# Performance work log

Hardware: AMD Instinct MI355X
Metric: run time of the kernel (lower is better)

The kernel has to match this reference:

```python
import jax, jax.numpy as jnp
import numpy as np
import math

NUM_HEADS = 8
LN_EPS = 1e-5


def layer_norm(x, g, b):
    mu = x.mean(-1, keepdims=True)
    var = ((x - mu) ** 2).mean(-1, keepdims=True)
    return (x - mu) * jax.lax.rsqrt(var + LN_EPS) * g + b


def typed_linear(x, W, types):
    # x: [E, in], W: [R, in, out], types: [E] int -> [E, out]
    out = jnp.zeros((x.shape[0], W.shape[-1]), x.dtype)
    for r in range(W.shape[0]):  # small fixed relation count
        out = out + jnp.where((types == r)[:, None], x @ W[r], 0.0)
    return out


def setup_inputs() -> dict:
    key = jax.random.key(0)
    ks = jax.random.split(key, 20)
    N, M, E = 50000, 10000, 100000
    in_dim, e_dim, out_dim, td = 128, 32, 128, 32
    R, T = 8, 4
    inp = {
        'src_h': jax.random.normal(ks[0], (N, in_dim), jnp.float32),
        'src_tw': jax.random.normal(ks[1], (N, td), jnp.float32),
        'src_tb': jax.random.normal(ks[2], (N, td), jnp.float32),
        'edge_h': jax.random.normal(ks[3], (E, e_dim), jnp.float32),
        'date': jax.random.uniform(ks[4], (E,), jnp.float32),
        'src_idx': jax.random.randint(ks[5], (E,), 0, N, jnp.int32),
        'dst_idx': jax.random.randint(ks[6], (E,), 0, M, jnp.int32),
        'etype': jax.random.randint(ks[7], (E,), 0, R, jnp.int32),
        'ntype': jax.random.randint(ks[8], (M,), 0, T, jnp.int32),
    }
    def w(k, shape):
        return jax.random.normal(k, shape, jnp.float32) / math.sqrt(shape[-2])
    inp['Wq'] = w(ks[9], (R, in_dim, out_dim))
    inp['Wk'] = w(ks[10], (R, in_dim + e_dim, out_dim))
    inp['Wv'] = w(ks[11], (R, in_dim + e_dim, out_dim))
    inp['Wa'] = w(ks[12], (T, out_dim, out_dim))
    inp['h_bias'] = jnp.zeros((T, out_dim), jnp.float32)
    inp['skip'] = jnp.ones((T,), jnp.float32)
    inp['src_ln_g'] = jnp.ones((in_dim + e_dim,), jnp.float32)
    inp['src_ln_b'] = jnp.zeros((in_dim + e_dim,), jnp.float32)
    inp['dst_ln_g'] = jnp.ones((in_dim,), jnp.float32)
    inp['dst_ln_b'] = jnp.zeros((in_dim,), jnp.float32)
    return inp


def reference(src_h, src_tw, src_tb, edge_h, date, src_idx, dst_idx, etype, ntype,
              Wq, Wk, Wv, Wa, h_bias, skip, src_ln_g, src_ln_b, dst_ln_g, dst_ln_b):
    M = ntype.shape[0]
    out_dim = Wq.shape[-1]
    H = NUM_HEADS
    hs = out_dim // H
    td = src_tw.shape[-1]
    t = date[:, None]  # [E,1]

    # gather src / dst node data per edge (dst nodes are first M src rows)
    h_s, tw_s, tb_s = src_h[src_idx], src_tw[src_idx], src_tb[src_idx]
    h_d, tw_d, tb_d = src_h[dst_idx], src_tw[dst_idx], src_tb[dst_idx]

    # time2vec modulation of the first td channels
    dia_s = jnp.concatenate([jnp.sin(tw_s * t + tb_s) * h_s[:, :td], h_s[:, td:]], -1)
    dia_d = jnp.concatenate([jnp.sin(tw_d * t + tb_d) * h_d[:, :td], h_d[:, td:]], -1)
    dia_s = jnp.concatenate([dia_s, edge_h], -1)  # [E, in_dim+e_dim]

    # pre_norm
    dia_s = layer_norm(dia_s, src_ln_g, src_ln_b)
    dia_d = layer_norm(dia_d, dst_ln_g, dst_ln_b)

    q = typed_linear(dia_d, Wq, etype).reshape(-1, H, hs)
    k = typed_linear(dia_s, Wk, etype).reshape(-1, H, hs)
    v = typed_linear(dia_s, Wv, etype).reshape(-1, H, hs)

    a = (q * k).sum(-1) / math.sqrt(out_dim)  # [E, H]

    # edge_softmax: segment softmax over destination nodes
    amax = jax.lax.stop_gradient(jax.ops.segment_max(a, dst_idx, num_segments=M))
    ex = jnp.exp(a - amax[dst_idx])
    denom = jax.ops.segment_sum(ex, dst_idx, num_segments=M)
    alpha = ex / denom[dst_idx]  # [E, H]

    # weighted scatter-sum aggregation
    m = (v * alpha[..., None]).reshape(-1, out_dim)  # [E, out_dim]
    h = jax.ops.segment_sum(m, dst_idx, num_segments=M)  # [M, out_dim]

    h = h + h_bias[ntype]
    gate = jax.nn.sigmoid(skip[ntype])[:, None]
    h = typed_linear(h, Wa, ntype)  # dropout is identity at eval
    dst_h = src_h[:M]
    return h * gate + dst_h * (1.0 - gate)
```

## Files before the change

### kernel.cpp

```cpp
#include <hip/hip_runtime.h>


typedef __attribute__((ext_vector_type(8))) short short8;
typedef __attribute__((ext_vector_type(4))) float f32x4;

__device__ __forceinline__ unsigned short f2bf(float f){
  union { float f; unsigned u; } x; x.f = f;
  unsigned r = x.u + 0x7FFFu + ((x.u >> 16) & 1u);
  return (unsigned short)(r >> 16);
}
__device__ __forceinline__ float bf2f(unsigned short b){
  union { unsigned u; float f; } x; x.u = ((unsigned)b) << 16;
  return x.f;
}


__global__ void k_zero(int* __restrict__ p, int n){
  int i = blockIdx.x*256 + threadIdx.x;
  if(i < n) p[i] = 0;
}

__global__ __launch_bounds__(256) void k_hist(
    const int* __restrict__ etype, const int* __restrict__ dst_idx,
    const int* __restrict__ ntype,
    int* cnt_e, int* cnt_d, int* cnt_n, int E, int M){
  __shared__ int le[8], ln[4];
  int tid = threadIdx.x;
  if(tid < 8) le[tid] = 0;
  if(tid < 4) ln[tid] = 0;
  __syncthreads();
  int g = blockIdx.x*256 + tid;
  if(g < E){ atomicAdd(&le[etype[g]], 1); atomicAdd(&cnt_d[dst_idx[g]], 1); }
  if(g < M){ atomicAdd(&ln[ntype[g]], 1); }
  __syncthreads();
  if(tid < 8 && le[tid]) atomicAdd(&cnt_e[tid], le[tid]);
  if(tid < 4 && ln[tid]) atomicAdd(&cnt_n[tid], ln[tid]);
}

__global__ __launch_bounds__(1024) void k_scan(const int* __restrict__ cnt_e, int* off_e,
                                               const int* __restrict__ cnt_n, int* off_n,
                                               const int* __restrict__ cnt_d, int* off_d, int M){
  __shared__ int part[1024];
  int tid = threadIdx.x;
  if(tid == 0){
    int s = 0;
    for(int i=0;i<8;i++){ off_e[i]=s; s+=cnt_e[i]; } off_e[8]=s;
    s = 0;
    for(int i=0;i<4;i++){ off_n[i]=s; s+=cnt_n[i]; } off_n[4]=s;
  }
  int per = (M + 1023) >> 10;
  int s = 0;
  for(int j=0;j<per;j++){ int idx = tid*per + j; if(idx < M) s += cnt_d[idx]; }
  part[tid] = s; __syncthreads();
  for(int o=1;o<1024;o<<=1){
    int v = (tid >= o) ? part[tid-o] : 0;
    __syncthreads();
    part[tid] += v;
    __syncthreads();
  }
  int run = (tid == 0) ? 0 : part[tid-1];
  for(int j=0;j<per;j++){
    int idx = tid*per + j;
    if(idx < M){ off_d[idx] = run; run += cnt_d[idx]; }
  }
  if(tid == 1023) off_d[M] = run;
}

__global__ __launch_bounds__(256) void k_scatter(
    const int* __restrict__ etype, const int* __restrict__ dst_idx,
    const int* __restrict__ ntype,
    const int* __restrict__ off_e, int* cur_e,
    const int* __restrict__ off_d, int* cur_d,
    const int* __restrict__ off_n, int* cur_n,
    int* eperm, int* dstlist, int* nperm, int* npos, int E, int M){
  __shared__ int lcnt[8], lbase[8], lnc[4], lnb[4];
  int tid = threadIdx.x;
  if(tid < 8) lcnt[tid] = 0;
  if(tid < 4) lnc[tid] = 0;
  __syncthreads();
  int g = blockIdx.x*256 + tid;
  int r = 0, lrank = 0, t = 0, nrank = 0;
  bool inE = (g < E), inM = (g < M);
  if(inE){ r = etype[g]; lrank = atomicAdd(&lcnt[r], 1); }
  if(inM){ t = ntype[g]; nrank = atomicAdd(&lnc[t], 1); }
  __syncthreads();
  if(tid < 8 && lcnt[tid]) lbase[tid] = atomicAdd(&cur_e[tid], lcnt[tid]);
  if(tid < 4 && lnc[tid])  lnb[tid]   = atomicAdd(&cur_n[tid], lnc[tid]);
  __syncthreads();
  if(inE){
    int p = off_e[r] + lbase[r] + lrank;
    eperm[p] = g;
    int d = dst_idx[g];
    int q = off_d[d] + atomicAdd(&cur_d[d], 1);
    dstlist[q] = p;
  }
  if(inM){
    int np = off_n[t] + lnb[t] + nrank;
    npos[g] = np;
    nperm[np] = g;
  }
}

__global__ void k_convw(const float* __restrict__ Wq, const float* __restrict__ Wk,
                        const float* __restrict__ Wv, const float* __restrict__ Wa,
                        unsigned short* Wq_t, unsigned short* Wk_t,
                        unsigned short* Wv_t, unsigned short* Wa_t){
  int tid = blockIdx.x*256 + threadIdx.x;
  if(tid < 131072){
    int r = tid >> 14, rem = tid & 16383, k = rem >> 7, n = rem & 127;
    int nb=n>>4, m=n&15, c=k>>5, quad=(k>>3)&3, j=k&7;
    Wq_t[r*16384 + ((nb*4 + c)*4 + quad)*128 + m*8 + j] = f2bf(Wq[tid]);
  } else if(tid < 294912){
    int u = tid - 131072;
    int r = u / 20480, rem = u - r*20480, k = rem >> 7, n = rem & 127;
    int nb=n>>4, m=n&15, c=k>>5, quad=(k>>3)&3, j=k&7;
    Wk_t[r*20480 + ((nb*5 + c)*4 + quad)*128 + m*8 + j] = f2bf(Wk[u]);
  } else if(tid < 458752){
    int u = tid - 294912;
    int r = u / 20480, rem = u - r*20480, k = rem >> 7, n = rem & 127;
    int nb=n>>4, m=n&15, c=k>>5, quad=(k>>3)&3, j=k&7;
    Wv_t[r*20480 + ((nb*5 + c)*4 + quad)*128 + m*8 + j] = f2bf(Wv[u]);
  } else if(tid < 524288){
    int u = tid - 458752;
    int r = u >> 14, rem = u & 16383, k = rem >> 7, n = rem & 127;
    int nb=n>>4, m=n&15, c=k>>5, quad=(k>>3)&3, j=k&7;
    Wa_t[r*16384 + ((nb*4 + c)*4 + quad)*128 + m*8 + j] = f2bf(Wa[u]);
  }
}

__global__ __launch_bounds__(256) void k_prep(
  const float* __restrict__ src_h, const float* __restrict__ src_tw, const float* __restrict__ src_tb,
  const float* __restrict__ edge_h, const float* __restrict__ date,
  const int* __restrict__ src_idx, const int* __restrict__ dst_idx, const int* __restrict__ eperm,
  const float* __restrict__ g_s, const float* __restrict__ b_s,
  const float* __restrict__ g_d, const float* __restrict__ b_d,
  unsigned short* __restrict__ dia_s, unsigned short* __restrict__ dia_d, int E)
{
  int p = blockIdx.x*8 + (threadIdx.x >> 5);
  if(p >= E) return;
  int l = threadIdx.x & 31;
  int e = eperm[p];
  float t = date[e];
  int s = src_idx[e], d = dst_idx[e];
  float4 hs = *(const float4*)(src_h + (size_t)s*128 + 4*l);
  float4 hd = *(const float4*)(src_h + (size_t)d*128 + 4*l);
  float xe = edge_h[(size_t)e*32 + l];
  float4 sx = hs, dx = hd;
  if(l < 8){
    float4 w4, c4;
    w4 = *(const float4*)(src_tw + (size_t)s*32 + 4*l);
    c4 = *(const float4*)(src_tb + (size_t)s*32 + 4*l);
    sx.x = __sinf(w4.x*t + c4.x) * hs.x;
    sx.y = __sinf(w4.y*t + c4.y) * hs.y;
    sx.z = __sinf(w4.z*t + c4.z) * hs.z;
    sx.w = __sinf(w4.w*t + c4.w) * hs.w;
    w4 = *(const float4*)(src_tw + (size_t)d*32 + 4*l);
    c4 = *(const float4*)(src_tb + (size_t)d*32 + 4*l);
    dx.x = __sinf(w4.x*t + c4.x) * hd.x;
    dx.y = __sinf(w4.y*t + c4.y) * hd.y;
    dx.z = __sinf(w4.z*t + c4.z) * hd.z;
    dx.w = __sinf(w4.w*t + c4.w) * hd.w;
  }
  float s1 = sx.x + sx.y + sx.z + sx.w + xe;
  float s2 = sx.x*sx.x + sx.y*sx.y + sx.z*sx.z + sx.w*sx.w + xe*xe;
  float t1 = dx.x + dx.y + dx.z + dx.w;
  float t2 = dx.x*dx.x + dx.y*dx.y + dx.z*dx.z + dx.w*dx.w;
  #pragma unroll
  for(int i=1;i<32;i<<=1){
    s1 += __shfl_xor(s1,i); s2 += __shfl_xor(s2,i);
    t1 += __shfl_xor(t1,i); t2 += __shfl_xor(t2,i);
  }
  float smu = s1*(1.f/160.f);
  float ssc = rsqrtf(s2*(1.f/160.f) - smu*smu + 1e-5f);
  float dmu = t1*(1.f/128.f);
  float dsc = rsqrtf(t2*(1.f/128.f) - dmu*dmu + 1e-5f);
  float4 gs = *(const float4*)(g_s + 4*l), bs = *(const float4*)(b_s + 4*l);
  float4 gd = *(const float4*)(g_d + 4*l), bd = *(const float4*)(b_d + 4*l);
  unsigned r0 = (unsigned)f2bf((sx.x-smu)*ssc*gs.x + bs.x)
              | ((unsigned)f2bf((sx.y-smu)*ssc*gs.y + bs.y) << 16);
  unsigned r1 = (unsigned)f2bf((sx.z-smu)*ssc*gs.z + bs.z)
              | ((unsigned)f2bf((sx.w-smu)*ssc*gs.w + bs.w) << 16);
  uint2 rs; rs.x = r0; rs.y = r1;
  *(uint2*)(dia_s + (size_t)p*160 + 4*l) = rs;
  dia_s[(size_t)p*160 + 128 + l] = f2bf((xe-smu)*ssc*g_s[128+l] + b_s[128+l]);
  unsigned d0 = (unsigned)f2bf((dx.x-dmu)*dsc*gd.x + bd.x)
              | ((unsigned)f2bf((dx.y-dmu)*dsc*gd.y + bd.y) << 16);
  unsigned d1 = (unsigned)f2bf((dx.z-dmu)*dsc*gd.z + bd.z)
              | ((unsigned)f2bf((dx.w-dmu)*dsc*gd.w + bd.w) << 16);
  uint2 rd; rd.x = d0; rd.y = d1;
  *(uint2*)(dia_d + (size_t)p*128 + 4*l) = rd;
}

template<int NC>
__device__ __forceinline__ void gemm64r(
  const unsigned short* __restrict__ A, int lda,
  const unsigned short* __restrict__ Wf,
  f32x4* acc, int tid)
{
  int lane = tid & 63, w = tid >> 6, m = lane & 15, quad = lane >> 4;
  const unsigned short* p0 = Wf + (size_t)(2*w)*NC*512 + lane*8;
  short8 b0[NC], b1[NC];
  #pragma unroll
  for(int c=0;c<NC;c++){
    b0[c] = *(const short8*)(p0 + c*512);
    b1[c] = *(const short8*)(p0 + NC*512 + c*512);
  }
  #pragma unroll
  for(int i=0;i<8;i++) acc[i] = (f32x4){0.f,0.f,0.f,0.f};
  #pragma unroll
  for(int c=0;c<NC;c++){
    #pragma unroll
    for(int rt=0; rt<4; rt++){
      short8 af = *(const short8*)(A + (rt*16 + m)*lda + c*32 + quad*8);
      acc[rt*2+0] = __builtin_amdgcn_mfma_f32_16x16x32_bf16(af, b0[c], acc[rt*2+0], 0,0,0);
      acc[rt*2+1] = __builtin_amdgcn_mfma_f32_16x16x32_bf16(af, b1[c], acc[rt*2+1], 0,0,0);
    }
  }
}

__global__ __launch_bounds__(256) void k_qkv(
  const unsigned short* __restrict__ dia_d, const unsigned short* __restrict__ dia_s,
  const unsigned short* __restrict__ Wq_t, const unsigned short* __restrict__ Wk_t,
  const unsigned short* __restrict__ Wv_t,
  const int* __restrict__ cnt_e, const int* __restrict__ off_e,
  float* __restrict__ abuf, unsigned short* __restrict__ vbuf)
{
  __shared__ unsigned short Ad[64*136];
  __shared__ unsigned short As[64*168];
  int bid = blockIdx.x;
  int r = -1, tl0 = 0, accT = 0;
  #pragma unroll
  for(int i=0;i<8;i++){
    int n = cnt_e[i], tt = (n + 63) >> 6;
    if(r < 0 && bid < accT + tt){ r = i; tl0 = bid - accT; }
    accT += tt;
  }
  if(r < 0) return;
  int row0 = off_e[r] + tl0*64;
  int nv = min(64, cnt_e[r] - tl0*64);
  int tid = threadIdx.x;
  {
    int4 z = make_int4(0,0,0,0);
    #pragma unroll
    for(int it=0; it<4; it++){
      int idx = it*256 + tid, row = idx >> 4, c = idx & 15;
      int4 v = z;
      if(row < nv) v = *(const int4*)(dia_d + (size_t)(row0+row)*128 + c*8);
      *(int4*)(Ad + row*136 + c*8) = v;
    }
    #pragma unroll
    for(int it=0; it<5; it++){
      int idx = it*256 + tid, row = idx/20, c = idx%20;
      int4 v = z;
      if(row < nv) v = *(const int4*)(dia_s + (size_t)(row0+row)*160 + c*8);
      *(int4*)(As + row*168 + c*8) = v;
    }
  }
  __syncthreads();
  int lane = tid & 63, w = tid >> 6, m = lane & 15, quad = lane >> 4;
  f32x4 q[8], kk[8], vv[8];
  gemm64r<4>(Ad, 136, Wq_t + r*16384, q,  tid);
  gemm64r<5>(As, 168, Wk_t + r*20480, kk, tid);
  const float inv = 0.08838834764831845f;
  #pragma unroll
  for(int rt=0; rt<4; rt++)
  #pragma unroll
  for(int ct=0; ct<2; ct++){
    #pragma unroll
    for(int reg=0; reg<4; reg++){
      float s = q[rt*2+ct][reg] * kk[rt*2+ct][reg];
      s += __shfl_xor(s,1); s += __shfl_xor(s,2); s += __shfl_xor(s,4); s += __shfl_xor(s,8);
      int row = rt*16 + quad*4 + reg;
      if(m == 0 && row < nv) abuf[(size_t)(row0+row)*8 + w*2 + ct] = s * inv;
    }
  }
  gemm64r<5>(As, 168, Wv_t + r*20480, vv, tid);
  #pragma unroll
  for(int rt=0; rt<4; rt++)
  #pragma unroll
  for(int ct=0; ct<2; ct++)
  #pragma unroll
  for(int reg=0; reg<4; reg++){
    int row = rt*16 + quad*4 + reg;
    if(row < nv)
      vbuf[(size_t)(row0+row)*128 + w*32 + ct*16 + m] = f2bf(vv[rt*2+ct][reg]);
  }
}

__global__ __launch_bounds__(128) void k_aggr(
  const float* __restrict__ abuf, const unsigned short* __restrict__ vbuf,
  const int* __restrict__ dstlist, const int* __restrict__ off_d,
  const int* __restrict__ npos, const int* __restrict__ ntype,
  const float* __restrict__ h_bias, unsigned short* __restrict__ hpre)
{
  int d = blockIdx.x, tid = threadIdx.x;
  int o0 = off_d[d], cnt = off_d[d+1] - o0;
  __shared__ float den[8];
  if(tid < 8) den[tid] = 0.f;
  __syncthreads();
  for(int idx = tid; idx < cnt*8; idx += 128){
    int i = idx >> 3, h = idx & 7;
    float ex = __expf(abuf[(size_t)dstlist[o0+i]*8 + h]);
    atomicAdd(&den[h], ex);
  }
  __syncthreads();
  int h = tid >> 4;
  float dh = den[h];
  float rd = (dh > 0.f) ? (1.f/dh) : 0.f;
  float acc = 0.f;
  for(int i=0; i<cnt; i++){
    int p = dstlist[o0+i];
    float al = __expf(abuf[(size_t)p*8 + h]) * rd;
    acc += al * bf2f(vbuf[(size_t)p*128 + tid]);
  }
  int t = ntype[d];
  acc += h_bias[t*128 + tid];
  hpre[(size_t)npos[d]*128 + tid] = f2bf(acc);
}

__global__ __launch_bounds__(256) void k_final(
  const unsigned short* __restrict__ hpre, const unsigned short* __restrict__ Wa_t,
  const int* __restrict__ cnt_n, const int* __restrict__ off_n, const int* __restrict__ nperm,
  const float* __restrict__ skip, const float* __restrict__ src_h, float* __restrict__ out)
{
  __shared__ unsigned short Ah[64*136];
  int bid = blockIdx.x;
  int r = -1, tl0 = 0, accT = 0;
  #pragma unroll
  for(int i=0;i<4;i++){
    int n = cnt_n[i], tt = (n + 63) >> 6;
    if(r < 0 && bid < accT + tt){ r = i; tl0 = bid - accT; }
    accT += tt;
  }
  if(r < 0) return;
  int row0 = off_n[r] + tl0*64;
  int nv = min(64, cnt_n[r] - tl0*64);
  float gate = 1.f / (1.f + __expf(-skip[r]));
  int tid = threadIdx.x;
  int4 z = make_int4(0,0,0,0);
  #pragma unroll
  for(int it=0; it<4; it++){
    int idx = it*256 + tid, row = idx >> 4, c = idx & 15;
    int4 v = z;
    if(row < nv) v = *(const int4*)(hpre + (size_t)(row0+row)*128 + c*8);
    *(int4*)(Ah + row*136 + c*8) = v;
  }
  __syncthreads();
  f32x4 acc[8];
  gemm64r<4>(Ah, 136, Wa_t + r*16384, acc, tid);
  int lane = tid & 63, w = tid >> 6, m = lane & 15, quad = lane >> 4;
  #pragma unroll
  for(int rt=0; rt<4; rt++)
  #pragma unroll
  for(int ct=0; ct<2; ct++)
  #pragma unroll
  for(int reg=0; reg<4; reg++){
    int row = rt*16 + quad*4 + reg;
    if(row < nv){
      int dd = nperm[row0+row];
      int col = w*32 + ct*16 + m;
      out[(size_t)dd*128 + col] = acc[rt*2+ct][reg]*gate + src_h[(size_t)dd*128 + col]*(1.f - gate);
    }
  }
}

extern "C" void kernel_launch(void* const* d_in, const int* in_sizes, int n_in,
                              void* d_out, int out_size, void* d_ws, size_t ws_size,
                              hipStream_t stream)
{
  const float* src_h  = (const float*)d_in[0];
  const float* src_tw = (const float*)d_in[1];
  const float* src_tb = (const float*)d_in[2];
  const float* edge_h = (const float*)d_in[3];
  const float* date   = (const float*)d_in[4];
  const int*   src_idx= (const int*)d_in[5];
  const int*   dst_idx= (const int*)d_in[6];
  const int*   etype  = (const int*)d_in[7];
  const int*   ntype  = (const int*)d_in[8];
  const float* Wq     = (const float*)d_in[9];
  const float* Wk     = (const float*)d_in[10];
  const float* Wv     = (const float*)d_in[11];
  const float* Wa     = (const float*)d_in[12];
  const float* h_bias = (const float*)d_in[13];
  const float* skip   = (const float*)d_in[14];
  const float* g_s    = (const float*)d_in[15];
  const float* b_s    = (const float*)d_in[16];
  const float* g_d    = (const float*)d_in[17];
  const float* b_d    = (const float*)d_in[18];
  float* out = (float*)d_out;

  const int E = in_sizes[4];
  const int M = in_sizes[8];

  char* base = (char*)d_ws;
  size_t off = 0;
  auto alloc = [&](size_t bytes)->char*{
    off = (off + 255) & ~(size_t)255;
    char* p = base + off; off += bytes; return p;
  };
  int* cnt_e = (int*)alloc((size_t)(24 + 2*M)*4);
  int* cur_e = cnt_e + 8;
  int* cnt_n = cur_e + 8;
  int* cur_n = cnt_n + 4;
  int* cnt_d = cur_n + 4;
  int* cur_d = cnt_d + M;
  const int nzero = 24 + 2*M;
  int* off_e = (int*)alloc(9*4);
  int* off_n = (int*)alloc(5*4);
  int* off_d = (int*)alloc((size_t)(M+1)*4);
  int* eperm   = (int*)alloc((size_t)E*4);
  int* dstlist = (int*)alloc((size_t)E*4);
  int* nperm   = (int*)alloc((size_t)M*4);
  int* npos    = (int*)alloc((size_t)M*4);
  unsigned short* Wq_t = (unsigned short*)alloc((size_t)8*128*128*2);
  unsigned short* Wk_t = (unsigned short*)alloc((size_t)8*160*128*2);
  unsigned short* Wv_t = (unsigned short*)alloc((size_t)8*160*128*2);
  unsigned short* Wa_t = (unsigned short*)alloc((size_t)4*128*128*2);
  unsigned short* dia_d = (unsigned short*)alloc((size_t)E*128*2);
  unsigned short* dia_s = (unsigned short*)alloc((size_t)E*160*2);
  unsigned short* vbuf  = (unsigned short*)alloc((size_t)E*128*2);
  unsigned short* hpre  = (unsigned short*)alloc((size_t)M*128*2);
  float* abuf = (float*)alloc((size_t)E*8*4);

  k_zero<<<dim3((nzero+255)/256), dim3(256), 0, stream>>>(cnt_e, nzero);
  k_hist<<<dim3((E+255)/256), dim3(256), 0, stream>>>(etype, dst_idx, ntype, cnt_e, cnt_d, cnt_n, E, M);
  k_scan<<<dim3(1), dim3(1024), 0, stream>>>(cnt_e, off_e, cnt_n, off_n, cnt_d, off_d, M);
  k_scatter<<<dim3((E+255)/256), dim3(256), 0, stream>>>(etype, dst_idx, ntype,
      off_e, cur_e, off_d, cur_d, off_n, cur_n, eperm, dstlist, nperm, npos, E, M);
  k_convw<<<dim3(2048), dim3(256), 0, stream>>>(Wq, Wk, Wv, Wa, Wq_t, Wk_t, Wv_t, Wa_t);
  k_prep<<<dim3((E+7)/8), dim3(256), 0, stream>>>(src_h, src_tw, src_tb, edge_h, date,
      src_idx, dst_idx, eperm, g_s, b_s, g_d, b_d, dia_s, dia_d, E);
  k_qkv<<<dim3(E/64 + 9), dim3(256), 0, stream>>>(dia_d, dia_s, Wq_t, Wk_t, Wv_t,
      cnt_e, off_e, abuf, vbuf);
  k_aggr<<<dim3(M), dim3(128), 0, stream>>>(abuf, vbuf, dstlist, off_d, npos, ntype, h_bias, hpre);
  k_final<<<dim3(M/64 + 5), dim3(256), 0, stream>>>(hpre, Wa_t, cnt_n, off_n, nperm, skip, src_h, out);
}
```

Before: 269.0 us.

## Split typed GEMMs across eight waves, one 16-column head per wave

The q/k/v and final typed-linear kernels move from 256 threads per 64-row tile to 512. Each of the eight waves now computes one 16-column slice (one attention head) instead of two. This halves the accumulator and weight registers per wave and doubles the waves available to hide MFMA and LDS latency. The cost is that the A-tile fragments in shared memory are read by twice as many waves, with less reuse of each A load per MFMA. The head score now goes straight to abuf at index w, since the wave index equals the head.

Measured after the change: 264.6 us. About the same (-1.7%).

```diff
diff --git a/kernel.cpp b/kernel.cpp
--- a/kernel.cpp
+++ b/kernel.cpp
@@ -192,33 +192,29 @@
 }
 
 template<int NC>
-__device__ __forceinline__ void gemm64r(
+__device__ __forceinline__ void gemm64r8(
   const unsigned short* __restrict__ A, int lda,
   const unsigned short* __restrict__ Wf,
   f32x4* acc, int tid)
 {
   int lane = tid & 63, w = tid >> 6, m = lane & 15, quad = lane >> 4;
-  const unsigned short* p0 = Wf + (size_t)(2*w)*NC*512 + lane*8;
-  short8 b0[NC], b1[NC];
-  #pragma unroll
-  for(int c=0;c<NC;c++){
-    b0[c] = *(const short8*)(p0 + c*512);
-    b1[c] = *(const short8*)(p0 + NC*512 + c*512);
-  }
-  #pragma unroll
-  for(int i=0;i<8;i++) acc[i] = (f32x4){0.f,0.f,0.f,0.f};
+  const unsigned short* p0 = Wf + (size_t)w*NC*512 + lane*8;
+  short8 b0[NC];
+  #pragma unroll
+  for(int c=0;c<NC;c++) b0[c] = *(const short8*)(p0 + c*512);
+  #pragma unroll
+  for(int i=0;i<4;i++) acc[i] = (f32x4){0.f,0.f,0.f,0.f};
   #pragma unroll
   for(int c=0;c<NC;c++){
     #pragma unroll
     for(int rt=0; rt<4; rt++){
       short8 af = *(const short8*)(A + (rt*16 + m)*lda + c*32 + quad*8);
-      acc[rt*2+0] = __builtin_amdgcn_mfma_f32_16x16x32_bf16(af, b0[c], acc[rt*2+0], 0,0,0);
-      acc[rt*2+1] = __builtin_amdgcn_mfma_f32_16x16x32_bf16(af, b1[c], acc[rt*2+1], 0,0,0);
+      acc[rt] = __builtin_amdgcn_mfma_f32_16x16x32_bf16(af, b0[c], acc[rt], 0,0,0);
     }
   }
 }
 
-__global__ __launch_bounds__(256) void k_qkv(
+__global__ __launch_bounds__(512) void k_qkv(
   const unsigned short* __restrict__ dia_d, const unsigned short* __restrict__ dia_s,
   const unsigned short* __restrict__ Wq_t, const unsigned short* __restrict__ Wk_t,
   const unsigned short* __restrict__ Wv_t,
@@ -242,48 +238,47 @@
   {
     int4 z = make_int4(0,0,0,0);
     #pragma unroll
-    for(int it=0; it<4; it++){
-      int idx = it*256 + tid, row = idx >> 4, c = idx & 15;
+    for(int it=0; it<2; it++){
+      int idx = it*512 + tid, row = idx >> 4, c = idx & 15;
       int4 v = z;
       if(row < nv) v = *(const int4*)(dia_d + (size_t)(row0+row)*128 + c*8);
       *(int4*)(Ad + row*136 + c*8) = v;
     }
     #pragma unroll
-    for(int it=0; it<5; it++){
-      int idx = it*256 + tid, row = idx/20, c = idx%20;
-      int4 v = z;
-      if(row < nv) v = *(const int4*)(dia_s + (size_t)(row0+row)*160 + c*8);
-      *(int4*)(As + row*168 + c*8) = v;
+    for(int it=0; it<3; it++){
+      int idx = it*512 + tid;
+      if(idx < 1280){
+        int row = idx/20, c = idx%20;
+        int4 v = z;
+        if(row < nv) v = *(const int4*)(dia_s + (size_t)(row0+row)*160 + c*8);
+        *(int4*)(As + row*168 + c*8) = v;
+      }
     }
   }
   __syncthreads();
   int lane = tid & 63, w = tid >> 6, m = lane & 15, quad = lane >> 4;
-  f32x4 q[8], kk[8], vv[8];
-  gemm64r<4>(Ad, 136, Wq_t + r*16384, q,  tid);
-  gemm64r<5>(As, 168, Wk_t + r*20480, kk, tid);
+  f32x4 q[4], kk[4], vv[4];
+  gemm64r8<4>(Ad, 136, Wq_t + r*16384, q,  tid);
+  gemm64r8<5>(As, 168, Wk_t + r*20480, kk, tid);
   const float inv = 0.08838834764831845f;
   #pragma unroll
-  for(int rt=0; rt<4; rt++)
-  #pragma unroll
-  for(int ct=0; ct<2; ct++){
+  for(int rt=0; rt<4; rt++){
     #pragma unroll
     for(int reg=0; reg<4; reg++){
-      float s = q[rt*2+ct][reg] * kk[rt*2+ct][reg];
+      float s = q[rt][reg] * kk[rt][reg];
       s += __shfl_xor(s,1); s += __shfl_xor(s,2); s += __shfl_xor(s,4); s += __shfl_xor(s,8);
       int row = rt*16 + quad*4 + reg;
-      if(m == 0 && row < nv) abuf[(size_t)(row0+row)*8 + w*2 + ct] = s * inv;
+      if(m == 0 && row < nv) abuf[(size_t)(row0+row)*8 + w] = s * inv;
     }
   }
-  gemm64r<5>(As, 168, Wv_t + r*20480, vv, tid);
+  gemm64r8<5>(As, 168, Wv_t + r*20480, vv, tid);
   #pragma unroll
   for(int rt=0; rt<4; rt++)
-  #pragma unroll
-  for(int ct=0; ct<2; ct++)
   #pragma unroll
   for(int reg=0; reg<4; reg++){
     int row = rt*16 + quad*4 + reg;
     if(row < nv)
-      vbuf[(size_t)(row0+row)*128 + w*32 + ct*16 + m] = f2bf(vv[rt*2+ct][reg]);
+      vbuf[(size_t)(row0+row)*128 + w*16 + m] = f2bf(vv[rt][reg]);
   }
 }
 
@@ -318,7 +313,7 @@
   hpre[(size_t)npos[d]*128 + tid] = f2bf(acc);
 }
 
-__global__ __launch_bounds__(256) void k_final(
+__global__ __launch_bounds__(512) void k_final(
   const unsigned short* __restrict__ hpre, const unsigned short* __restrict__ Wa_t,
   const int* __restrict__ cnt_n, const int* __restrict__ off_n, const int* __restrict__ nperm,
   const float* __restrict__ skip, const float* __restrict__ src_h, float* __restrict__ out)
@@ -339,27 +334,25 @@
   int tid = threadIdx.x;
   int4 z = make_int4(0,0,0,0);
   #pragma unroll
-  for(int it=0; it<4; it++){
-    int idx = it*256 + tid, row = idx >> 4, c = idx & 15;
+  for(int it=0; it<2; it++){
+    int idx = it*512 + tid, row = idx >> 4, c = idx & 15;
     int4 v = z;
     if(row < nv) v = *(const int4*)(hpre + (size_t)(row0+row)*128 + c*8);
     *(int4*)(Ah + row*136 + c*8) = v;
   }
   __syncthreads();
-  f32x4 acc[8];
-  gemm64r<4>(Ah, 136, Wa_t + r*16384, acc, tid);
+  f32x4 acc[4];
+  gemm64r8<4>(Ah, 136, Wa_t + r*16384, acc, tid);
   int lane = tid & 63, w = tid >> 6, m = lane & 15, quad = lane >> 4;
   #pragma unroll
   for(int rt=0; rt<4; rt++)
-  #pragma unroll
-  for(int ct=0; ct<2; ct++)
   #pragma unroll
   for(int reg=0; reg<4; reg++){
     int row = rt*16 + quad*4 + reg;
     if(row < nv){
       int dd = nperm[row0+row];
-      int col = w*32 + ct*16 + m;
-      out[(size_t)dd*128 + col] = acc[rt*2+ct][reg]*gate + src_h[(size_t)dd*128 + col]*(1.f - gate);
+      int col = w*16 + m;
+      out[(size_t)dd*128 + col] = acc[rt][reg]*gate + src_h[(size_t)dd*128 + col]*(1.f - gate);
     }
   }
 }
@@ -430,8 +423,8 @@
   k_convw<<<dim3(2048), dim3(256), 0, stream>>>(Wq, Wk, Wv, Wa, Wq_t, Wk_t, Wv_t, Wa_t);
   k_prep<<<dim3((E+7)/8), dim3(256), 0, stream>>>(src_h, src_tw, src_tb, edge_h, date,
       src_idx, dst_idx, eperm, g_s, b_s, g_d, b_d, dia_s, dia_d, E);
-  k_qkv<<<dim3(E/64 + 9), dim3(256), 0, stream>>>(dia_d, dia_s, Wq_t, Wk_t, Wv_t,
+  k_qkv<<<dim3(E/64 + 9), dim3(512), 0, stream>>>(dia_d, dia_s, Wq_t, Wk_t, Wv_t,
       cnt_e, off_e, abuf, vbuf);
   k_aggr<<<dim3(M), dim3(128), 0, stream>>>(abuf, vbuf, dstlist, off_d, npos, ntype, h_bias, hpre);
-  k_final<<<dim3(M/64 + 5), dim3(256), 0, stream>>>(hpre, Wa_t, cnt_n, off_n, nperm, skip, src_h, out);
-}
+  k_final<<<dim3(M/64 + 5), dim3(512), 0, stream>>>(hpre, Wa_t, cnt_n, off_n, nperm, skip, src_h, out);
+}
```
